# Kernel optimization log

Hardware: AMD Instinct MI355X
Metric: run time of the kernel (lower is better)

Reference implementation:

```python
import jax, jax.numpy as jnp
import numpy as np

EPS = 1e-6


def rms_norm(x, w):
    xf = x.astype(jnp.float32)
    var = jnp.mean(xf * xf, axis=-1, keepdims=True)
    return (xf * jax.lax.rsqrt(var + EPS)).astype(x.dtype) * w


def rope_interleaved(x, cos, sin):
    # x: [B, S, D]; rotate interleaved pairs (even=real, odd=imag)
    B, S, D = x.shape
    xp = x.reshape(B, S, D // 2, 2)
    rot = jnp.stack([-xp[..., 1], xp[..., 0]], axis=-1).reshape(B, S, D)
    return (x.astype(jnp.float32) * cos + rot.astype(jnp.float32) * sin).astype(x.dtype)


def setup_inputs() -> dict:
    key = jax.random.key(0)
    ks = jax.random.split(key, 8)
    B, S, D = 1, 2048, 2048
    H, Dh = 32, 64
    std = 1.0 / np.sqrt(D)

    hidden_states = jax.random.normal(ks[0], (B, S, D), jnp.float32)

    # interleaved RoPE tables tiled across heads -> [1, S, D]
    pos = np.arange(S, dtype=np.float64)
    inv_freq = 1.0 / (10000.0 ** (np.arange(0, Dh, 2, dtype=np.float64) / Dh))
    ang = pos[:, None] * inv_freq[None, :]          # [S, Dh/2]
    ang = np.repeat(ang, 2, axis=-1)                 # [S, Dh] interleaved
    ang = np.tile(ang, (1, H))                       # [S, D]
    cos = jnp.asarray(np.cos(ang)[None], jnp.float32)
    sin = jnp.asarray(np.sin(ang)[None], jnp.float32)

    Wq = jax.random.normal(ks[1], (D, D), jnp.float32) * std
    Wk = jax.random.normal(ks[2], (D, D), jnp.float32) * std
    Wv = jax.random.normal(ks[3], (D, D), jnp.float32) * std
    Wo = jax.random.normal(ks[4], (D, D), jnp.float32) * std
    bq = jax.random.normal(ks[5], (D,), jnp.float32) * 0.02
    bk = jax.random.normal(ks[6], (D,), jnp.float32) * 0.02
    bv = jax.random.normal(ks[7], (D,), jnp.float32) * 0.02
    bo = jnp.zeros((D,), jnp.float32)
    q_norm_w = jnp.ones((D,), jnp.float32)
    k_norm_w = jnp.ones((D,), jnp.float32)
    return {
        "hidden_states": hidden_states, "cos": cos, "sin": sin,
        "Wq": Wq, "bq": bq, "Wk": Wk, "bk": bk, "Wv": Wv, "bv": bv,
        "q_norm_w": q_norm_w, "k_norm_w": k_norm_w, "Wo": Wo, "bo": bo,
    }


def reference(hidden_states, cos, sin, Wq, bq, Wk, bk, Wv, bv, q_norm_w, k_norm_w, Wo, bo):
    B, S, D = hidden_states.shape
    H, Dh = 32, 64
    # QKV projections (self-attention: encoder_hidden_states = hidden_states)
    q = hidden_states @ Wq + bq
    k = hidden_states @ Wk + bk
    v = hidden_states @ Wv + bv
    # RMSNorm across heads (over full inner_dim)
    q = rms_norm(q, q_norm_w)
    k = rms_norm(k, k_norm_w)
    # interleaved rotary embedding (key uses query rope when key rope is None)
    q = rope_interleaved(q, cos, sin)
    k = rope_interleaved(k, cos, sin)
    # split heads: [B, H, S, Dh]
    q = q.reshape(B, S, H, Dh).transpose(0, 2, 1, 3)
    k = k.reshape(B, S, H, Dh).transpose(0, 2, 1, 3)
    v = v.reshape(B, S, H, Dh).transpose(0, 2, 1, 3)
    # scaled dot-product attention (no mask, not causal)
    scale = 1.0 / jnp.sqrt(jnp.asarray(Dh, q.dtype))
    scores = jnp.einsum("bhqd,bhkd->bhqk", q, k) * scale
    attn = jax.nn.softmax(scores, axis=-1)
    out = jnp.einsum("bhqk,bhkd->bhqd", attn, v)
    out = out.transpose(0, 2, 1, 3).reshape(B, S, H * Dh)
    return out @ Wo + bo
```

## Files before the change

kernel.cpp:

```cpp
#include <hip/hip_runtime.h>
#include <hip/hip_bf16.h>

typedef __bf16 bf16_t;
typedef __bf16 bf16x8 __attribute__((ext_vector_type(8)));
typedef __bf16 bf16x4 __attribute__((ext_vector_type(4)));
typedef float floatx4 __attribute__((ext_vector_type(4)));
typedef float floatx16 __attribute__((ext_vector_type(16)));

#define S_LEN 2048
#define D_DIM 2048
#define NHEADS 32
#define DH 64

__device__ __forceinline__ void gll16(const bf16_t* g, bf16_t* l) {
    __builtin_amdgcn_global_load_lds(
        (const __attribute__((address_space(1))) unsigned int*)g,
        (__attribute__((address_space(3))) unsigned int*)l, 16, 0, 0);
}

__global__ __launch_bounds__(256) void k_cvt_bf16(const float* __restrict__ x,
                                                  bf16_t* __restrict__ y, int n) {
    int i = (blockIdx.x * 256 + threadIdx.x) * 8;
    if (i + 8 > n) return;
    const float4 a = *(const float4*)(x + i);
    const float4 b = *(const float4*)(x + i + 4);
    bf16x8 o;
    o[0] = (bf16_t)a.x; o[1] = (bf16_t)a.y; o[2] = (bf16_t)a.z; o[3] = (bf16_t)a.w;
    o[4] = (bf16_t)b.x; o[5] = (bf16_t)b.y; o[6] = (bf16_t)b.z; o[7] = (bf16_t)b.w;
    *(bf16x8*)(y + i) = o;
}

__global__ __launch_bounds__(256) void k_transpose4(
    const float* __restrict__ W0, const float* __restrict__ W1,
    const float* __restrict__ W2, const float* __restrict__ W3,
    bf16_t* __restrict__ T0, bf16_t* __restrict__ T1,
    bf16_t* __restrict__ T2, bf16_t* __restrict__ T3)
{
    const float* W; bf16_t* T;
    switch (blockIdx.z) {
        case 0: W = W0; T = T0; break;
        case 1: W = W1; T = T1; break;
        case 2: W = W2; T = T2; break;
        default: W = W3; T = T3; break;
    }
    __shared__ float tile[64][65];
    const int n0 = blockIdx.x * 64, k0 = blockIdx.y * 64;
    const int tx = threadIdx.x & 63, ty = threadIdx.x >> 6;
    #pragma unroll
    for (int i = 0; i < 16; ++i) {
        int r = i * 4 + ty;
        tile[r][tx] = W[(size_t)(k0 + r) * D_DIM + n0 + tx];
    }
    __syncthreads();
    #pragma unroll
    for (int i = 0; i < 16; ++i) {
        int r = i * 4 + ty;
        T[(size_t)(n0 + r) * D_DIM + k0 + tx] = (bf16_t)tile[tx][r];
    }
}

#define BM 128
#define BN 128
#define BK 32

__global__ __launch_bounds__(256) void k_gemm_bt(
    const bf16_t* __restrict__ A,
    const bf16_t* __restrict__ Bt0, const bf16_t* __restrict__ Bt1, const bf16_t* __restrict__ Bt2,
    const float* __restrict__ bias0, const float* __restrict__ bias1, const float* __restrict__ bias2,
    float* __restrict__ C0, float* __restrict__ C1, bf16_t* __restrict__ VtOut,
    int M, int N, int K)
{
    const bf16_t* Bt; const float* bias;
    if (blockIdx.z == 0)      { Bt = Bt0; bias = bias0; }
    else if (blockIdx.z == 1) { Bt = Bt1; bias = bias1; }
    else                      { Bt = Bt2; bias = bias2; }

    __shared__ bf16_t As[BM][BK];
    __shared__ bf16_t Bs[BN][BK];

    const int t    = threadIdx.x;
    const int lane = t & 63;
    const int wave = t >> 6;
    const int wm = (wave >> 1) * 64;
    const int wn = (wave & 1) * 64;
    const int bm = blockIdx.y * BM;
    const int bn = blockIdx.x * BN;
    const int lm = lane & 15;
    const int lq = lane >> 4;

    const int srow0 = wave * 32 + (lane >> 2);
    const int srow1 = srow0 + 16;
    const int cp    = lane & 3;
    const int gc0 = cp ^ ((srow0 >> 1) & 3);
    const int gc1 = cp ^ ((srow1 >> 1) & 3);

    const bf16_t* Ag0 = A  + (size_t)(bm + srow0) * K + gc0 * 8;
    const bf16_t* Ag1 = A  + (size_t)(bm + srow1) * K + gc1 * 8;
    const bf16_t* Bg0 = Bt + (size_t)(bn + srow0) * K + gc0 * 8;
    const bf16_t* Bg1 = Bt + (size_t)(bn + srow1) * K + gc1 * 8;
    bf16_t* Al0 = &As[wave * 32][0];
    bf16_t* Al1 = &As[wave * 32 + 16][0];
    bf16_t* Bl0 = &Bs[wave * 32][0];
    bf16_t* Bl1 = &Bs[wave * 32 + 16][0];

    floatx4 acc[4][4];
    #pragma unroll
    for (int i = 0; i < 4; ++i)
        #pragma unroll
        for (int j = 0; j < 4; ++j)
            #pragma unroll
            for (int r = 0; r < 4; ++r) acc[i][j][r] = 0.f;

    for (int k0 = 0; k0 < K; k0 += BK) {
        __syncthreads();
        gll16(Ag0 + k0, Al0);
        gll16(Ag1 + k0, Al1);
        gll16(Bg0 + k0, Bl0);
        gll16(Bg1 + k0, Bl1);
        __syncthreads();

        bf16x8 af[4], bfr[4];
        #pragma unroll
        for (int i = 0; i < 4; ++i) {
            const int row = wm + i * 16 + lm;
            af[i] = *(const bf16x8*)&As[row][(lq ^ ((row >> 1) & 3)) * 8];
        }
        #pragma unroll
        for (int j = 0; j < 4; ++j) {
            const int row = wn + j * 16 + lm;
            bfr[j] = *(const bf16x8*)&Bs[row][(lq ^ ((row >> 1) & 3)) * 8];
        }
        #pragma unroll
        for (int i = 0; i < 4; ++i)
            #pragma unroll
            for (int j = 0; j < 4; ++j)
                acc[i][j] = __builtin_amdgcn_mfma_f32_16x16x32_bf16(af[i], bfr[j], acc[i][j], 0, 0, 0);
    }

    if (blockIdx.z == 2) {
        #pragma unroll
        for (int i = 0; i < 4; ++i) {
            const int row0 = bm + wm + i * 16 + lq * 4;
            #pragma unroll
            for (int j = 0; j < 4; ++j) {
                const int col = bn + wn + j * 16 + lm;
                const float bb = bias[col];
                bf16x4 pk;
                #pragma unroll
                for (int r = 0; r < 4; ++r) pk[r] = (bf16_t)(acc[i][j][r] + bb);
                *(bf16x4*)(VtOut + (size_t)col * M + row0) = pk;
            }
        }
    } else {
        float* C = (blockIdx.z == 0) ? C0 : C1;
        #pragma unroll
        for (int i = 0; i < 4; ++i) {
            const int row0 = bm + wm + i * 16 + lq * 4;
            #pragma unroll
            for (int j = 0; j < 4; ++j) {
                const int col = bn + wn + j * 16 + lm;
                const float bb = bias[col];
                #pragma unroll
                for (int r = 0; r < 4; ++r)
                    C[(size_t)(row0 + r) * N + col] = acc[i][j][r] + bb;
            }
        }
    }
}

__global__ __launch_bounds__(256) void k_norm_rope(
    const float* __restrict__ Qf, const float* __restrict__ Kf,
    bf16_t* __restrict__ Qb, bf16_t* __restrict__ Kb,
    const float* __restrict__ qw, const float* __restrict__ kw,
    const float* __restrict__ cosb, const float* __restrict__ sinb)
{
    const float* X = (blockIdx.z == 0) ? Qf : Kf;
    bf16_t* Y = (blockIdx.z == 0) ? Qb : Kb;
    const float* w = (blockIdx.z == 0) ? qw : kw;
    const int row = blockIdx.x;
    const int t = threadIdx.x;
    const size_t base = (size_t)row * D_DIM + t * 8;

    float x[8];
    { float4 a = *(const float4*)(X + base); float4 b = *(const float4*)(X + base + 4);
      x[0]=a.x; x[1]=a.y; x[2]=a.z; x[3]=a.w; x[4]=b.x; x[5]=b.y; x[6]=b.z; x[7]=b.w; }

    float ss = 0.f;
    #pragma unroll
    for (int i = 0; i < 8; ++i) ss += x[i] * x[i];
    #pragma unroll
    for (int off = 32; off; off >>= 1) ss += __shfl_xor(ss, off);
    __shared__ float red[4];
    if ((t & 63) == 0) red[t >> 6] = ss;
    __syncthreads();
    const float tot = red[0] + red[1] + red[2] + red[3];
    const float rms = rsqrtf(tot * (1.0f / D_DIM) + 1e-6f);

    float wv[8], c[8], sn[8];
    { float4 a = *(const float4*)(w + t * 8); float4 b = *(const float4*)(w + t * 8 + 4);
      wv[0]=a.x; wv[1]=a.y; wv[2]=a.z; wv[3]=a.w; wv[4]=b.x; wv[5]=b.y; wv[6]=b.z; wv[7]=b.w; }
    { float4 a = *(const float4*)(cosb + base); float4 b = *(const float4*)(cosb + base + 4);
      c[0]=a.x; c[1]=a.y; c[2]=a.z; c[3]=a.w; c[4]=b.x; c[5]=b.y; c[6]=b.z; c[7]=b.w; }
    { float4 a = *(const float4*)(sinb + base); float4 b = *(const float4*)(sinb + base + 4);
      sn[0]=a.x; sn[1]=a.y; sn[2]=a.z; sn[3]=a.w; sn[4]=b.x; sn[5]=b.y; sn[6]=b.z; sn[7]=b.w; }

    bf16x8 o;
    #pragma unroll
    for (int p = 0; p < 4; ++p) {
        const float e  = x[2*p]     * rms * wv[2*p];
        const float od = x[2*p + 1] * rms * wv[2*p + 1];
        o[2*p]     = (bf16_t)(e * c[2*p]     - od * sn[2*p]);
        o[2*p + 1] = (bf16_t)(od * c[2*p + 1] + e * sn[2*p + 1]);
    }
    *(bf16x8*)(Y + base) = o;
}

#define LDPQ 72

__global__ __launch_bounds__(256) void k_flash(
    const bf16_t* __restrict__ Qb, const bf16_t* __restrict__ Kb,
    const bf16_t* __restrict__ Vt, bf16_t* __restrict__ Ob)
{
    const int h = blockIdx.y, hc = h * DH;
    const int t = threadIdx.x;
    const int wave = t >> 6, lane = t & 63;
    const int ln = lane & 31, hf = lane >> 5;
    const int qw = blockIdx.x * 128 + wave * 32;

    __shared__ bf16_t Ks[64][64];
    __shared__ bf16_t Vs[64][64];
    __shared__ bf16_t Ps[4][32][LDPQ];

    bf16x8 bq[4];
    #pragma unroll
    for (int kt = 0; kt < 4; ++kt)
        bq[kt] = *(const bf16x8*)(Qb + (size_t)(qw + ln) * D_DIM + hc + kt * 16 + hf * 8);

    const int r0  = wave * 16 + (lane >> 3);
    const int r1  = r0 + 8;
    const int cp8 = lane & 7;
    const int gc0 = cp8 ^ (r0 & 7);
    const int gc1 = cp8 ^ (r1 & 7);
    const bf16_t* kg0 = Kb + (size_t)r0 * D_DIM + hc + gc0 * 8;
    const bf16_t* kg1 = Kb + (size_t)r1 * D_DIM + hc + gc1 * 8;
    const bf16_t* vg0 = Vt + (size_t)(hc + r0) * S_LEN + gc0 * 8;
    const bf16_t* vg1 = Vt + (size_t)(hc + r1) * S_LEN + gc1 * 8;
    bf16_t* kl0 = &Ks[wave * 16][0];
    bf16_t* kl1 = &Ks[wave * 16 + 8][0];
    bf16_t* vl0 = &Vs[wave * 16][0];
    bf16_t* vl1 = &Vs[wave * 16 + 8][0];

    floatx16 o0, o1, lf;
    #pragma unroll
    for (int r = 0; r < 16; ++r) { o0[r] = 0.f; o1[r] = 0.f; lf[r] = 0.f; }

    bf16x8 ones;
    #pragma unroll
    for (int j = 0; j < 8; ++j) ones[j] = (bf16_t)1.0f;

    const int swz = ln & 7;
    const float c_exp = 0.125f * 1.44269504089f;

    for (int kc = 0; kc < S_LEN; kc += 64) {
        __syncthreads();
        gll16(kg0 + (size_t)kc * D_DIM, kl0);
        gll16(kg1 + (size_t)kc * D_DIM, kl1);
        gll16(vg0 + kc, vl0);
        gll16(vg1 + kc, vl1);
        __syncthreads();

        floatx16 st0, st1;
        #pragma unroll
        for (int r = 0; r < 16; ++r) { st0[r] = 0.f; st1[r] = 0.f; }
        #pragma unroll
        for (int kt = 0; kt < 4; ++kt) {
            const int ch = 2 * kt + hf;
            const bf16x8 a0 = *(const bf16x8*)&Ks[ln]     [(ch ^ swz) * 8];
            const bf16x8 a1 = *(const bf16x8*)&Ks[32 + ln][(ch ^ swz) * 8];
            st0 = __builtin_amdgcn_mfma_f32_32x32x16_bf16(a0, bq[kt], st0, 0, 0, 0);
            st1 = __builtin_amdgcn_mfma_f32_32x32x16_bf16(a1, bq[kt], st1, 0, 0, 0);
        }

        #pragma unroll
        for (int g = 0; g < 4; ++g) {
            bf16x4 p0, p1;
            #pragma unroll
            for (int r4 = 0; r4 < 4; ++r4) {
                p0[r4] = (bf16_t)__builtin_amdgcn_exp2f(st0[4 * g + r4] * c_exp);
                p1[r4] = (bf16_t)__builtin_amdgcn_exp2f(st1[4 * g + r4] * c_exp);
            }
            *(bf16x4*)&Ps[wave][ln][8 * g + 4 * hf]      = p0;
            *(bf16x4*)&Ps[wave][ln][32 + 8 * g + 4 * hf] = p1;
        }
        asm volatile("s_waitcnt lgkmcnt(0)" ::: "memory");

        #pragma unroll
        for (int kt = 0; kt < 4; ++kt) {
            const int ch = 2 * kt + hf;
            const bf16x8 ap  = *(const bf16x8*)&Ps[wave][ln][kt * 16 + hf * 8];
            const bf16x8 bv0 = *(const bf16x8*)&Vs[ln]     [(ch ^ swz) * 8];
            const bf16x8 bv1 = *(const bf16x8*)&Vs[32 + ln][(ch ^ swz) * 8];
            o0 = __builtin_amdgcn_mfma_f32_32x32x16_bf16(ap, bv0, o0, 0, 0, 0);
            o1 = __builtin_amdgcn_mfma_f32_32x32x16_bf16(ap, bv1, o1, 0, 0, 0);
            lf = __builtin_amdgcn_mfma_f32_32x32x16_bf16(ap, ones, lf, 0, 0, 0);
        }
    }

    #pragma unroll
    for (int r = 0; r < 16; ++r) {
        const int row = (r & 3) + 8 * (r >> 2) + 4 * hf;
        const float inv = 1.0f / lf[r];
        Ob[(size_t)(qw + row) * D_DIM + hc + ln]      = (bf16_t)(o0[r] * inv);
        Ob[(size_t)(qw + row) * D_DIM + hc + 32 + ln] = (bf16_t)(o1[r] * inv);
    }
}

extern "C" void kernel_launch(void* const* d_in, const int* in_sizes, int n_in,
                              void* d_out, int out_size, void* d_ws, size_t ws_size,
                              hipStream_t stream) {
    const float* hs   = (const float*)d_in[0];
    const float* cosb = (const float*)d_in[1];
    const float* sinb = (const float*)d_in[2];
    const float* Wq   = (const float*)d_in[3];
    const float* bq   = (const float*)d_in[4];
    const float* Wk   = (const float*)d_in[5];
    const float* bk   = (const float*)d_in[6];
    const float* Wv   = (const float*)d_in[7];
    const float* bv   = (const float*)d_in[8];
    const float* qw   = (const float*)d_in[9];
    const float* kw   = (const float*)d_in[10];
    const float* Wo   = (const float*)d_in[11];
    const float* bo   = (const float*)d_in[12];
    float* out = (float*)d_out;

    char* ws = (char*)d_ws;
    bf16_t* Xb  = (bf16_t*)(ws);
    bf16_t* Wqt = (bf16_t*)(ws + ((size_t)8  << 20));
    bf16_t* Wkt = (bf16_t*)(ws + ((size_t)16 << 20));
    bf16_t* Wvt = (bf16_t*)(ws + ((size_t)24 << 20));
    bf16_t* Wot = (bf16_t*)(ws + ((size_t)32 << 20));
    float*  Qf  = (float*) (ws + ((size_t)40 << 20));
    float*  Kf  = (float*) (ws + ((size_t)56 << 20));
    bf16_t* Vt  = (bf16_t*)(ws + ((size_t)72 << 20));
    bf16_t* Qb  = (bf16_t*)(ws);
    bf16_t* Kb  = (bf16_t*)(ws + ((size_t)8  << 20));
    bf16_t* Ob  = (bf16_t*)(ws + ((size_t)16 << 20));

    const int n = S_LEN * D_DIM;

    k_cvt_bf16<<<n / (256 * 8), 256, 0, stream>>>(hs, Xb, n);
    k_transpose4<<<dim3(32, 32, 4), 256, 0, stream>>>(Wq, Wk, Wv, Wo, Wqt, Wkt, Wvt, Wot);

    k_gemm_bt<<<dim3(D_DIM / BN, S_LEN / BM, 3), 256, 0, stream>>>(
        Xb, Wqt, Wkt, Wvt, bq, bk, bv, Qf, Kf, Vt, S_LEN, D_DIM, D_DIM);

    k_norm_rope<<<dim3(S_LEN, 1, 2), 256, 0, stream>>>(Qf, Kf, Qb, Kb, qw, kw, cosb, sinb);

    k_flash<<<dim3(S_LEN / 128, NHEADS), 256, 0, stream>>>(Qb, Kb, Vt, Ob);

    k_gemm_bt<<<dim3(D_DIM / BN, S_LEN / BM, 1), 256, 0, stream>>>(
        Ob, Wot, Wot, Wot, bo, bo, bo, out, out, (bf16_t*)nullptr, S_LEN, D_DIM, D_DIM);
}
```

Measured before the change: 370.8 us.

## Multi-buffer GEMM and flash loads, split-K the output projection

Adds a triple-buffered global-to-LDS pipeline to the QKV GEMM and a double-buffered K/V pipeline to the flash attention kernel, using explicit vmcnt waits so loads overlap MFMA work. The output projection, which previously ran only 256 blocks, is split three ways along K into fp32 partial buffers, followed by a reduce kernel that adds the bias. This is meant to hide load latency and fill more CUs, at the cost of extra LDS per block and extra partial-sum memory traffic plus one more launch.

```diff
diff --git a/kernel.cpp b/kernel.cpp
--- a/kernel.cpp
+++ b/kernel.cpp
@@ -17,6 +17,9 @@
         (const __attribute__((address_space(1))) unsigned int*)g,
         (__attribute__((address_space(3))) unsigned int*)l, 16, 0, 0);
 }
+
+#define BAR()    asm volatile("s_barrier" ::: "memory")
+#define WAIT(N)  asm volatile("s_waitcnt vmcnt(" #N ")" ::: "memory")
 
 __global__ __launch_bounds__(256) void k_cvt_bf16(const float* __restrict__ x,
                                                   bf16_t* __restrict__ y, int n) {
@@ -63,7 +66,7 @@
 #define BN 128
 #define BK 32
 
-__global__ __launch_bounds__(256) void k_gemm_bt(
+__global__ __launch_bounds__(256) void k_gemm_qkv(
     const bf16_t* __restrict__ A,
     const bf16_t* __restrict__ Bt0, const bf16_t* __restrict__ Bt1, const bf16_t* __restrict__ Bt2,
     const float* __restrict__ bias0, const float* __restrict__ bias1, const float* __restrict__ bias2,
@@ -75,8 +78,8 @@
     else if (blockIdx.z == 1) { Bt = Bt1; bias = bias1; }
     else                      { Bt = Bt2; bias = bias2; }
 
-    __shared__ bf16_t As[BM][BK];
-    __shared__ bf16_t Bs[BN][BK];
+    __shared__ bf16_t As[3][BM][BK];
+    __shared__ bf16_t Bs[3][BN][BK];
 
     const int t    = threadIdx.x;
     const int lane = t & 63;
@@ -98,10 +101,6 @@
     const bf16_t* Ag1 = A  + (size_t)(bm + srow1) * K + gc1 * 8;
     const bf16_t* Bg0 = Bt + (size_t)(bn + srow0) * K + gc0 * 8;
     const bf16_t* Bg1 = Bt + (size_t)(bn + srow1) * K + gc1 * 8;
-    bf16_t* Al0 = &As[wave * 32][0];
-    bf16_t* Al1 = &As[wave * 32 + 16][0];
-    bf16_t* Bl0 = &Bs[wave * 32][0];
-    bf16_t* Bl1 = &Bs[wave * 32 + 16][0];
 
     floatx4 acc[4][4];
     #pragma unroll
@@ -111,30 +110,45 @@
             #pragma unroll
             for (int r = 0; r < 4; ++r) acc[i][j][r] = 0.f;
 
-    for (int k0 = 0; k0 < K; k0 += BK) {
-        __syncthreads();
-        gll16(Ag0 + k0, Al0);
-        gll16(Ag1 + k0, Al1);
-        gll16(Bg0 + k0, Bl0);
-        gll16(Bg1 + k0, Bl1);
-        __syncthreads();
-
+    const int NIT = K / BK;
+    auto stage = [&](int buf, int k0) {
+        gll16(Ag0 + k0, &As[buf][wave * 32][0]);
+        gll16(Ag1 + k0, &As[buf][wave * 32 + 16][0]);
+        gll16(Bg0 + k0, &Bs[buf][wave * 32][0]);
+        gll16(Bg1 + k0, &Bs[buf][wave * 32 + 16][0]);
+    };
+    stage(0, 0);
+    stage(1, BK);
+
+    for (int i = 0; i < NIT; ++i) {
+        BAR();
+        if (i + 2 < NIT) {
+            stage((i + 2) % 3, (i + 2) * BK);
+            WAIT(8);
+        } else if (i + 1 < NIT) {
+            WAIT(4);
+        } else {
+            WAIT(0);
+        }
+        BAR();
+
+        const int buf = i % 3;
         bf16x8 af[4], bfr[4];
         #pragma unroll
-        for (int i = 0; i < 4; ++i) {
-            const int row = wm + i * 16 + lm;
-            af[i] = *(const bf16x8*)&As[row][(lq ^ ((row >> 1) & 3)) * 8];
+        for (int ii = 0; ii < 4; ++ii) {
+            const int row = wm + ii * 16 + lm;
+            af[ii] = *(const bf16x8*)&As[buf][row][(lq ^ ((row >> 1) & 3)) * 8];
         }
         #pragma unroll
         for (int j = 0; j < 4; ++j) {
             const int row = wn + j * 16 + lm;
-            bfr[j] = *(const bf16x8*)&Bs[row][(lq ^ ((row >> 1) & 3)) * 8];
-        }
-        #pragma unroll
-        for (int i = 0; i < 4; ++i)
+            bfr[j] = *(const bf16x8*)&Bs[buf][row][(lq ^ ((row >> 1) & 3)) * 8];
+        }
+        #pragma unroll
+        for (int ii = 0; ii < 4; ++ii)
             #pragma unroll
             for (int j = 0; j < 4; ++j)
-                acc[i][j] = __builtin_amdgcn_mfma_f32_16x16x32_bf16(af[i], bfr[j], acc[i][j], 0, 0, 0);
+                acc[ii][j] = __builtin_amdgcn_mfma_f32_16x16x32_bf16(af[ii], bfr[j], acc[ii][j], 0, 0, 0);
     }
 
     if (blockIdx.z == 2) {
@@ -166,6 +180,121 @@
             }
         }
     }
+}
+
+__global__ __launch_bounds__(256) void k_gemm_splitk(
+    const bf16_t* __restrict__ A, const bf16_t* __restrict__ Bt,
+    float* __restrict__ Cpart, int M, int N, int K)
+{
+    __shared__ bf16_t As[3][BM][BK];
+    __shared__ bf16_t Bs[3][BN][BK];
+
+    const int t    = threadIdx.x;
+    const int lane = t & 63;
+    const int wave = t >> 6;
+    const int wm = (wave >> 1) * 64;
+    const int wn = (wave & 1) * 64;
+    const int bm = blockIdx.y * BM;
+    const int bn = blockIdx.x * BN;
+    const int lm = lane & 15;
+    const int lq = lane >> 4;
+    const int z  = blockIdx.z;
+
+    const int nit_all = K / BK;
+    const int it0 = (z * nit_all) / 3;
+    const int it1 = ((z + 1) * nit_all) / 3;
+    const int NIT = it1 - it0;
+    const int kbase = it0 * BK;
+
+    const int srow0 = wave * 32 + (lane >> 2);
+    const int srow1 = srow0 + 16;
+    const int cp    = lane & 3;
+    const int gc0 = cp ^ ((srow0 >> 1) & 3);
+    const int gc1 = cp ^ ((srow1 >> 1) & 3);
+
+    const bf16_t* Ag0 = A  + (size_t)(bm + srow0) * K + kbase + gc0 * 8;
+    const bf16_t* Ag1 = A  + (size_t)(bm + srow1) * K + kbase + gc1 * 8;
+    const bf16_t* Bg0 = Bt + (size_t)(bn + srow0) * K + kbase + gc0 * 8;
+    const bf16_t* Bg1 = Bt + (size_t)(bn + srow1) * K + kbase + gc1 * 8;
+
+    floatx4 acc[4][4];
+    #pragma unroll
+    for (int i = 0; i < 4; ++i)
+        #pragma unroll
+        for (int j = 0; j < 4; ++j)
+            #pragma unroll
+            for (int r = 0; r < 4; ++r) acc[i][j][r] = 0.f;
+
+    auto stage = [&](int buf, int k0) {
+        gll16(Ag0 + k0, &As[buf][wave * 32][0]);
+        gll16(Ag1 + k0, &As[buf][wave * 32 + 16][0]);
+        gll16(Bg0 + k0, &Bs[buf][wave * 32][0]);
+        gll16(Bg1 + k0, &Bs[buf][wave * 32 + 16][0]);
+    };
+    stage(0, 0);
+    if (1 < NIT) stage(1, BK);
+
+    for (int i = 0; i < NIT; ++i) {
+        BAR();
+        if (i + 2 < NIT) {
+            stage((i + 2) % 3, (i + 2) * BK);
+            WAIT(8);
+        } else if (i + 1 < NIT) {
+            WAIT(4);
+        } else {
+            WAIT(0);
+        }
+        BAR();
+
+        const int buf = i % 3;
+        bf16x8 af[4], bfr[4];
+        #pragma unroll
+        for (int ii = 0; ii < 4; ++ii) {
+            const int row = wm + ii * 16 + lm;
+            af[ii] = *(const bf16x8*)&As[buf][row][(lq ^ ((row >> 1) & 3)) * 8];
+        }
+        #pragma unroll
+        for (int j = 0; j < 4; ++j) {
+            const int row = wn + j * 16 + lm;
+            bfr[j] = *(const bf16x8*)&Bs[buf][row][(lq ^ ((row >> 1) & 3)) * 8];
+        }
+        #pragma unroll
+        for (int ii = 0; ii < 4; ++ii)
+            #pragma unroll
+            for (int j = 0; j < 4; ++j)
+                acc[ii][j] = __builtin_amdgcn_mfma_f32_16x16x32_bf16(af[ii], bfr[j], acc[ii][j], 0, 0, 0);
+    }
+
+    float* C = Cpart + (size_t)z * M * N;
+    #pragma unroll
+    for (int i = 0; i < 4; ++i) {
+        const int row0 = bm + wm + i * 16 + lq * 4;
+        #pragma unroll
+        for (int j = 0; j < 4; ++j) {
+            const int col = bn + wn + j * 16 + lm;
+            #pragma unroll
+            for (int r = 0; r < 4; ++r)
+                C[(size_t)(row0 + r) * N + col] = acc[i][j][r];
+        }
+    }
+}
+
+__global__ __launch_bounds__(256) void k_reduce_bias(
+    const float* __restrict__ P, const float* __restrict__ bias,
+    float* __restrict__ out)
+{
+    const int i = (blockIdx.x * 256 + threadIdx.x) * 4;
+    const size_t NN = (size_t)S_LEN * D_DIM;
+    const float4 b  = *(const float4*)(bias + (i & (D_DIM - 1)));
+    const float4 a0 = *(const float4*)(P + i);
+    const float4 a1 = *(const float4*)(P + NN + i);
+    const float4 a2 = *(const float4*)(P + 2 * NN + i);
+    float4 o;
+    o.x = b.x + a0.x + a1.x + a2.x;
+    o.y = b.y + a0.y + a1.y + a2.y;
+    o.z = b.z + a0.z + a1.z + a2.z;
+    o.w = b.w + a0.w + a1.w + a2.w;
+    *(float4*)(out + i) = o;
 }
 
 __global__ __launch_bounds__(256) void k_norm_rope(
@@ -227,8 +356,8 @@
     const int ln = lane & 31, hf = lane >> 5;
     const int qw = blockIdx.x * 128 + wave * 32;
 
-    __shared__ bf16_t Ks[64][64];
-    __shared__ bf16_t Vs[64][64];
+    __shared__ bf16_t Ks[2][64][64];
+    __shared__ bf16_t Vs[2][64][64];
     __shared__ bf16_t Ps[4][32][LDPQ];
 
     bf16x8 bq[4];
@@ -239,16 +368,19 @@
     const int r0  = wave * 16 + (lane >> 3);
     const int r1  = r0 + 8;
     const int cp8 = lane & 7;
-    const int gc0 = cp8 ^ (r0 & 7);
-    const int gc1 = cp8 ^ (r1 & 7);
-    const bf16_t* kg0 = Kb + (size_t)r0 * D_DIM + hc + gc0 * 8;
-    const bf16_t* kg1 = Kb + (size_t)r1 * D_DIM + hc + gc1 * 8;
-    const bf16_t* vg0 = Vt + (size_t)(hc + r0) * S_LEN + gc0 * 8;
-    const bf16_t* vg1 = Vt + (size_t)(hc + r1) * S_LEN + gc1 * 8;
-    bf16_t* kl0 = &Ks[wave * 16][0];
-    bf16_t* kl1 = &Ks[wave * 16 + 8][0];
-    bf16_t* vl0 = &Vs[wave * 16][0];
-    bf16_t* vl1 = &Vs[wave * 16 + 8][0];
+    const int gcA = cp8 ^ (r0 & 7);
+    const int gcB = cp8 ^ (r1 & 7);
+    const bf16_t* kg0 = Kb + (size_t)r0 * D_DIM + hc + gcA * 8;
+    const bf16_t* kg1 = Kb + (size_t)r1 * D_DIM + hc + gcB * 8;
+    const bf16_t* vg0 = Vt + (size_t)(hc + r0) * S_LEN + gcA * 8;
+    const bf16_t* vg1 = Vt + (size_t)(hc + r1) * S_LEN + gcB * 8;
+
+    auto stageKV = [&](int buf, int kc) {
+        gll16(kg0 + (size_t)kc * D_DIM, &Ks[buf][wave * 16][0]);
+        gll16(kg1 + (size_t)kc * D_DIM, &Ks[buf][wave * 16 + 8][0]);
+        gll16(vg0 + kc, &Vs[buf][wave * 16][0]);
+        gll16(vg1 + kc, &Vs[buf][wave * 16 + 8][0]);
+    };
 
     floatx16 o0, o1, lf;
     #pragma unroll
@@ -261,13 +393,18 @@
     const int swz = ln & 7;
     const float c_exp = 0.125f * 1.44269504089f;
 
+    stageKV(0, 0);
+
     for (int kc = 0; kc < S_LEN; kc += 64) {
-        __syncthreads();
-        gll16(kg0 + (size_t)kc * D_DIM, kl0);
-        gll16(kg1 + (size_t)kc * D_DIM, kl1);
-        gll16(vg0 + kc, vl0);
-        gll16(vg1 + kc, vl1);
-        __syncthreads();
+        const int cur = (kc >> 6) & 1;
+        BAR();
+        if (kc + 64 < S_LEN) {
+            stageKV(cur ^ 1, kc + 64);
+            WAIT(4);
+        } else {
+            WAIT(0);
+        }
+        BAR();
 
         floatx16 st0, st1;
         #pragma unroll
@@ -275,8 +412,8 @@
         #pragma unroll
         for (int kt = 0; kt < 4; ++kt) {
             const int ch = 2 * kt + hf;
-            const bf16x8 a0 = *(const bf16x8*)&Ks[ln]     [(ch ^ swz) * 8];
-            const bf16x8 a1 = *(const bf16x8*)&Ks[32 + ln][(ch ^ swz) * 8];
+            const bf16x8 a0 = *(const bf16x8*)&Ks[cur][ln]     [(ch ^ swz) * 8];
+            const bf16x8 a1 = *(const bf16x8*)&Ks[cur][32 + ln][(ch ^ swz) * 8];
             st0 = __builtin_amdgcn_mfma_f32_32x32x16_bf16(a0, bq[kt], st0, 0, 0, 0);
             st1 = __builtin_amdgcn_mfma_f32_32x32x16_bf16(a1, bq[kt], st1, 0, 0, 0);
         }
@@ -298,8 +435,8 @@
         for (int kt = 0; kt < 4; ++kt) {
             const int ch = 2 * kt + hf;
             const bf16x8 ap  = *(const bf16x8*)&Ps[wave][ln][kt * 16 + hf * 8];
-            const bf16x8 bv0 = *(const bf16x8*)&Vs[ln]     [(ch ^ swz) * 8];
-            const bf16x8 bv1 = *(const bf16x8*)&Vs[32 + ln][(ch ^ swz) * 8];
+            const bf16x8 bv0 = *(const bf16x8*)&Vs[cur][ln]     [(ch ^ swz) * 8];
+            const bf16x8 bv1 = *(const bf16x8*)&Vs[cur][32 + ln][(ch ^ swz) * 8];
             o0 = __builtin_amdgcn_mfma_f32_32x32x16_bf16(ap, bv0, o0, 0, 0, 0);
             o1 = __builtin_amdgcn_mfma_f32_32x32x16_bf16(ap, bv1, o1, 0, 0, 0);
             lf = __builtin_amdgcn_mfma_f32_32x32x16_bf16(ap, ones, lf, 0, 0, 0);
@@ -345,19 +482,21 @@
     bf16_t* Qb  = (bf16_t*)(ws);
     bf16_t* Kb  = (bf16_t*)(ws + ((size_t)8  << 20));
     bf16_t* Ob  = (bf16_t*)(ws + ((size_t)16 << 20));
+    float*  Pp  = (float*) (ws + ((size_t)40 << 20));
 
     const int n = S_LEN * D_DIM;
 
     k_cvt_bf16<<<n / (256 * 8), 256, 0, stream>>>(hs, Xb, n);
     k_transpose4<<<dim3(32, 32, 4), 256, 0, stream>>>(Wq, Wk, Wv, Wo, Wqt, Wkt, Wvt, Wot);
 
-    k_gemm_bt<<<dim3(D_DIM / BN, S_LEN / BM, 3), 256, 0, stream>>>(
+    k_gemm_qkv<<<dim3(D_DIM / BN, S_LEN / BM, 3), 256, 0, stream>>>(
         Xb, Wqt, Wkt, Wvt, bq, bk, bv, Qf, Kf, Vt, S_LEN, D_DIM, D_DIM);
 
     k_norm_rope<<<dim3(S_LEN, 1, 2), 256, 0, stream>>>(Qf, Kf, Qb, Kb, qw, kw, cosb, sinb);
 
     k_flash<<<dim3(S_LEN / 128, NHEADS), 256, 0, stream>>>(Qb, Kb, Vt, Ob);
 
-    k_gemm_bt<<<dim3(D_DIM / BN, S_LEN / BM, 1), 256, 0, stream>>>(
-        Ob, Wot, Wot, Wot, bo, bo, bo, out, out, (bf16_t*)nullptr, S_LEN, D_DIM, D_DIM);
-}
+    k_gemm_splitk<<<dim3(D_DIM / BN, S_LEN / BM, 3), 256, 0, stream>>>(
+        Ob, Wot, Pp, S_LEN, D_DIM, D_DIM);
+    k_reduce_bias<<<n / (256 * 4), 256, 0, stream>>>(Pp, bo, out);
+}
```

After: 357.7 us. 3.5% less time.
